# Optimization experiments

Hardware: AMD Instinct MI355X
Metric: run time of the kernel (lower is better)

Reference implementation:

```python
import jax, jax.numpy as jnp
import numpy as np

B, N, K = 64, 1024, 20
HEADS, DIM_K, DIM_V, CH_RAISE = 8, 32, 32, 64
C_CAT = 4 * 2 + DIM_V  # 44


def setup_inputs() -> dict:
    key = jax.random.key(0)
    ks = jax.random.split(key, 16)

    def w(k, shape):
        fan_in = shape[-1]
        return jax.random.normal(k, shape, dtype=jnp.float32) / np.sqrt(fan_in)

    def gamma(k, n):
        return 1.0 + 0.1 * jax.random.normal(k, (n,), dtype=jnp.float32)

    def beta(k, n):
        return 0.1 * jax.random.normal(k, (n,), dtype=jnp.float32)

    return {
        "x": jax.random.normal(ks[0], (B, N, 4), dtype=jnp.float32),
        "W_h": w(ks[1], (DIM_V, 4)),              # mlp_h: conv2d 4 -> dim_v, 1x1
        "W1": w(ks[2], (CH_RAISE, C_CAT)),        # mlp conv2d 44 -> 64
        "g1": gamma(ks[3], CH_RAISE), "b1": beta(ks[4], CH_RAISE),
        "W2": w(ks[5], (CH_RAISE, CH_RAISE)),     # mlp conv2d 64 -> 64
        "g2": gamma(ks[6], CH_RAISE), "b2": beta(ks[7], CH_RAISE),
        "W_v": w(ks[8], (DIM_V, C_CAT)),          # mlp_v conv1d 44 -> 32
        "gv": gamma(ks[9], DIM_V), "bv": beta(ks[10], DIM_V),
        "W_k": w(ks[11], (DIM_K, C_CAT)),         # mlp_k conv1d 44 -> 32
        "W_q": w(ks[12], (HEADS * DIM_K, CH_RAISE)),  # mlp_q conv1d 64 -> 256
        "gq": gamma(ks[13], HEADS * DIM_K), "bq": beta(ks[14], HEADS * DIM_K),
    }


def _forward(x, W_h, W1, g1, b1, W2, g2, b2, W_v, gv, bv, W_k, W_q, gq, bq):
    xyz = x[..., :4]                 # [B,N,4]
    feat = xyz                       # use_norm=False -> feature = xyz
    b, n, _ = xyz.shape

    # squared pairwise distances [B,N,N]
    sq = jnp.sum(xyz * xyz, axis=-1)
    dist = -2.0 * jnp.einsum('bnc,bmc->bnm', xyz, xyz) + sq[:, :, None] + sq[:, None, :]

    # KNN: K smallest distances
    _, knn_idx = jax.lax.top_k(-dist, K)          # [B,N,K]
    bidx = jnp.arange(b)[:, None, None]
    neighbor_xyz = xyz[bidx, knn_idx]             # [B,N,K,4]
    grouped = feat[bidx, knn_idx]                 # [B,N,K,4]

    feat_t = jnp.transpose(feat, (0, 2, 1))       # [B,4,N]
    grouped_c = jnp.transpose(grouped, (0, 3, 1, 2))          # [B,4,N,K]
    gnorm = grouped_c - feat_t[..., None]                     # [B,4,N,K]
    rel = jnp.transpose(neighbor_xyz - xyz[:, :, None, :], (0, 3, 1, 2))  # [B,4,N,K]

    pos = jnp.einsum('vc,bcnk->bvnk', W_h, rel)               # [B,32,N,K]
    center = jnp.broadcast_to(feat_t[..., None], (b, 4, n, K))
    feature = jnp.concatenate([gnorm, center, pos], axis=1)   # [B,44,N,K]

    # mlp: two 1x1 conv + BN(eval, affine) + ReLU
    h = jnp.einsum('oc,bcnk->bonk', W1, feature)
    h = jax.nn.relu(g1[None, :, None, None] * h + b1[None, :, None, None])
    h = jnp.einsum('oc,bcnk->bonk', W2, h)
    h = jax.nn.relu(g2[None, :, None, None] * h + b2[None, :, None, None])
    feature_q = jnp.max(h, axis=-1)                           # [B,64,N]

    q = jnp.einsum('oc,bcn->bon', W_q, feature_q)             # [B,256,N]
    q = jax.nn.relu(gq[None, :, None] * q + bq[None, :, None])
    q = q.reshape(b, HEADS, DIM_K, n)                         # [B,h,d,N]

    v = jnp.einsum('vc,bcnk->bvnk', W_v, feature)             # [B,32,N,K]
    v = gv[None, :, None, None] * v + bv[None, :, None, None]
    v = jnp.transpose(v, (0, 2, 1, 3))                        # [B,N,v,K]

    kk = jnp.einsum('dc,bcnk->bdnk', W_k, feature)            # [B,32,N,K]
    kk = jax.nn.softmax(kk, axis=-1)
    kk = jnp.transpose(kk, (0, 2, 1, 3))                      # [B,N,d,K]

    kv = jnp.einsum('bndk,bnvk->bdvn', kk, v)                 # [B,d,v,N]
    out = jnp.einsum('bhdn,bdvn->bhvn', q, kv)                # [B,h,v,N]
    out = out.reshape(b, HEADS * DIM_V, n)                    # [B,256,N]
    return xyz, out


def reference(x, W_h, W1, g1, b1, W2, g2, b2, W_v, gv, bv, W_k, W_q, gq, bq):
    return _forward(x, W_h, W1, g1, b1, W2, g2, b2, W_v, gv, bv, W_k, W_q, gq, bq)
```

## Files before the change

### kernel.cpp

```cpp
#include <hip/hip_runtime.h>
#include <math.h>

#define NPTS 1024
#define KNBR 20
#define CH 64


typedef __attribute__((ext_vector_type(8))) short s16x8;
typedef __attribute__((ext_vector_type(4))) float f32x4;

static __device__ __forceinline__ ushort f2bf(float f) {
  uint u = __float_as_uint(f);
  uint r = (u + 0x7FFFu + ((u >> 16) & 1u)) >> 16;
  return (ushort)r;
}

static __device__ __forceinline__ uint pkbf(float a, float b) {
  uint ua = __float_as_uint(a) + 0x8000u;
  uint ub = __float_as_uint(b) + 0x8000u;
  return __builtin_amdgcn_perm(ub, ua, 0x07060302);
}

static __device__ __forceinline__ int mbcnt64(unsigned long long m) {
  return __builtin_amdgcn_mbcnt_hi((uint)(m >> 32),
                                   __builtin_amdgcn_mbcnt_lo((uint)m, 0));
}

__global__ __launch_bounds__(256) void k_prep(
    const float* __restrict__ Wh, const float* __restrict__ W1,
    const float* __restrict__ g1, const float* __restrict__ b1,
    const float* __restrict__ Wv, const float* __restrict__ Wk,
    const float* __restrict__ W2, const float* __restrict__ Wq,
    float* __restrict__ wp, ushort* __restrict__ w2b,
    ushort* __restrict__ wqb, ushort* __restrict__ w1b) {
  int t = threadIdx.x;
  {
    int o = t >> 2, c = t & 3;
    float acc = W1[o * 40 + c];
    #pragma unroll
    for (int v = 0; v < 32; ++v) acc = fmaf(W1[o * 40 + 8 + v], Wh[v * 4 + c], acc);
    float g = g1[o];
    wp[t] = g * acc;
    wp[256 + t] = g * W1[o * 40 + 4 + c];
  }
  if (t < 128) {
    int d = t >> 2, c = t & 3;
    float av = Wv[d * 40 + c];
    float ak = Wk[d * 40 + c];
    #pragma unroll
    for (int u = 0; u < 32; ++u) {
      av = fmaf(Wv[d * 40 + 8 + u], Wh[u * 4 + c], av);
      ak = fmaf(Wk[d * 40 + 8 + u], Wh[u * 4 + c], ak);
    }
    wp[512 + t] = av;
    wp[640 + t] = Wv[d * 40 + 4 + c];
    wp[768 + t] = ak;
    wp[896 + t] = Wk[d * 40 + 4 + c];
  }
  #pragma unroll
  for (int i = 0; i < 16; ++i) w2b[t * 16 + i] = f2bf(W2[t * 16 + i]);
  for (int i = 0; i < 64; ++i) wqb[t * 64 + i] = f2bf(Wq[t * 64 + i]);
  __syncthreads();
  for (int idx = t; idx < 2048; idx += 256) {
    int ch = idx >> 5, kk = idx & 31;
    float v = 0.f;
    if (kk < 4) v = wp[ch * 4 + kk];
    else if (kk < 8) v = wp[256 + ch * 4 + (kk - 4)];
    else if (kk == 8) v = b1[ch];
    w1b[idx] = f2bf(v);
  }
}

__global__ __launch_bounds__(256) void k_knn(const float4* __restrict__ xv,
                                             ushort* __restrict__ knn,
                                             float4* __restrict__ outx) {
  __shared__ float4 sx[NPTS];
  __shared__ float ssq[NPTS];
  __shared__ uint s_sk[4][64];
  __shared__ ushort s_sj[4][64];

  int t = threadIdx.x;
  int b = blockIdx.x >> 6, grp = blockIdx.x & 63;
  for (int j = t; j < NPTS; j += 256) {
    float4 p = xv[b * NPTS + j];
    sx[j] = p;
    ssq[j] = p.x * p.x + p.y * p.y + p.z * p.z + p.w * p.w;
    if (grp == 0) outx[b * NPTS + j] = p;
  }
  __syncthreads();

  int w = t >> 6, l = t & 63;

  #pragma unroll 1
  for (int i = 0; i < 4; ++i) {
    int cloc = grp * 16 + w * 4 + i;
    int gid20 = (b * NPTS + cloc) * KNBR;
    float4 c = sx[cloc];
    uint u[16];
    uint mn = 0xFFFFFFFFu;
    #pragma unroll
    for (int s = 0; s < 16; ++s) {
      int j = s * 64 + l;
      float4 q = sx[j];
      float dot = c.x * q.x;
      dot = fmaf(c.y, q.y, dot);
      dot = fmaf(c.z, q.z, dot);
      dot = fmaf(c.w, q.w, dot);
      float key = fmaf(-2.f, dot, ssq[j]);
      uint uu = __float_as_uint(key);
      uu = ((int)uu < 0) ? ~uu : (uu | 0x80000000u);
      u[s] = uu;
      mn = min(mn, uu);
    }

    uint T0 = 0;
    #pragma unroll
    for (int bit = 31; bit >= 0; --bit) {
      uint cand = T0 | (1u << bit);
      if (__popcll(__ballot(mn < cand)) < 20) T0 = cand;
    }

    int base = 0;
    #pragma unroll
    for (int s = 0; s < 16; ++s) {
      unsigned long long mask = __ballot(u[s] <= T0);
      if (u[s] <= T0) {
        int off = base + mbcnt64(mask);
        if (off < 64) {
          s_sk[w][off] = u[s];
          s_sj[w][off] = (ushort)(s * 64 + l);
        }
      }
      base += (int)__popcll(mask);
    }
    int scnt = base;

    if (scnt <= 64) {
      asm volatile("s_waitcnt lgkmcnt(0)" ::: "memory");
      __builtin_amdgcn_sched_barrier(0);
      uint uk = (l < scnt) ? s_sk[w][l] : 0xFFFFFFFFu;
      uint uj = (l < scnt) ? (uint)s_sj[w][l] : 0xFFFFu;

      uint u20 = 0;
      #pragma unroll
      for (int bit = 31; bit >= 0; --bit) {
        uint cand = u20 | (1u << bit);
        if (__popcll(__ballot(uk < cand)) < 20) u20 = cand;
      }
      int m = (int)__popcll(__ballot(uk < u20));
      int r = 20 - m;
      uint jr = 0;
      #pragma unroll
      for (int bit = 10; bit >= 0; --bit) {
        uint cand = jr | (1u << bit);
        if (__popcll(__ballot((uk == u20) && (uj < cand))) < r) jr = cand;
      }
      bool sel = (uk < u20) || ((uk == u20) && (uj <= jr));
      unsigned long long smask = __ballot(sel);
      int off = mbcnt64(smask);
      if (sel) knn[gid20 + off] = (ushort)uj;
    } else {
      uint u20 = 0;
      #pragma unroll 1
      for (int bit = 31; bit >= 0; --bit) {
        uint cand = u20 | (1u << bit);
        int cnt2 = 0;
        #pragma unroll
        for (int s = 0; s < 16; ++s)
          cnt2 += (int)__popcll(__ballot(u[s] < cand));
        if (cnt2 < 20) u20 = cand;
      }
      int base2 = 0;
      #pragma unroll
      for (int s = 0; s < 16; ++s) {
        unsigned long long mask = __ballot(u[s] < u20);
        if (u[s] < u20) knn[gid20 + base2 + mbcnt64(mask)] = (ushort)(s * 64 + l);
        base2 += (int)__popcll(mask);
      }
      int r = 20 - base2;
      #pragma unroll
      for (int s = 0; s < 16; ++s) {
        unsigned long long mask = __ballot(u[s] == u20);
        int pos = mbcnt64(mask);
        int cntm = (int)__popcll(mask);
        int take = (r < cntm) ? r : cntm;
        if ((u[s] == u20) && (pos < take))
          knn[gid20 + base2 + pos] = (ushort)(s * 64 + l);
        base2 += take;
        r -= take;
      }
    }
  }
}

__global__ __launch_bounds__(256) void k_fused(
    const float4* __restrict__ xv, const ushort* __restrict__ knn,
    const float* __restrict__ wp, const ushort* __restrict__ w1b,
    const ushort* __restrict__ w2b, const ushort* __restrict__ wqb,
    const float* __restrict__ g2, const float* __restrict__ b2,
    const float* __restrict__ gq, const float* __restrict__ bq,
    const float* __restrict__ gv, const float* __restrict__ bv,
    float* __restrict__ o1) {
  __shared__ __align__(16) char smem[51200];
  char* s_h1 = smem;
  ushort* s_qb = (ushort*)smem;
  ushort* s_eb = (ushort*)(smem + 10496);
  float* s_out = (float*)(smem + 10496);
  float4* s_rel = (float4*)(smem + 40960);
  char* s_fqb = smem + 46080;
  float4* s_ctr = (float4*)(smem + 48384);
  ushort* s_ab = (ushort*)(smem + 40960);

  int t = threadIdx.x;
  int gid0 = blockIdx.x * 16;
  int bbase = (gid0 >> 10) << 10;
  int b = gid0 >> 10;
  int n0 = gid0 & 1023;
  int w = t >> 6, l = t & 63;
  int g = l >> 4, lane16 = l & 15;

  if (t < 16) s_ctr[t] = xv[gid0 + t];
  #pragma unroll
  for (int it2 = 0; it2 < 2; ++it2) {
    int idx = t + it2 * 256;
    if (idx < 320) {
      int p = (int)(((uint)idx * 3277u) >> 16);
      int k = idx - p * 20;
      int nb = (int)knn[(size_t)(gid0 + p) * KNBR + k];
      float4 nx = xv[bbase + nb];
      float4 ct = xv[gid0 + p];
      s_rel[p * 20 + k] =
          make_float4(nx.x - ct.x, nx.y - ct.y, nx.z - ct.z, nx.w - ct.w);
    }
  }
  __syncthreads();

  {
    s16x8 ah[4];
    #pragma unroll
    for (int m = 0; m < 4; ++m)
      ah[m] = *(const s16x8*)(w1b + (m * 16 + lane16) * 32 + g * 8);
    s16x8 bz = {0, 0, 0, 0, 0, 0, 0, 0};
    s16x8 bone = bz;
    bone[0] = (short)0x3F80;
    #pragma unroll
    for (int q = 0; q < 5; ++q) {
      int col = w * 80 + q * 16 + lane16;
      s16x8 bf;
      if (g == 0) {
        float4 r = s_rel[lane16 * 20 + 5 * w + q];
        float4 ct = s_ctr[lane16];
        union { uint4 u; s16x8 s; } cv;
        cv.u.x = pkbf(r.x, r.y);
        cv.u.y = pkbf(r.z, r.w);
        cv.u.z = pkbf(ct.x, ct.y);
        cv.u.w = pkbf(ct.z, ct.w);
        bf = cv.s;
      } else {
        bf = (g == 1) ? bone : bz;
      }
      int swz = (col & 7) << 4;
      #pragma unroll
      for (int m = 0; m < 4; ++m) {
        f32x4 acc = {0.f, 0.f, 0.f, 0.f};
        acc = __builtin_amdgcn_mfma_f32_16x16x32_bf16(ah[m], bf, acc, 0, 0, 0);
        uint2 hv;
        hv.x = pkbf(fmaxf(acc[0], 0.f), fmaxf(acc[1], 0.f));
        hv.y = pkbf(fmaxf(acc[2], 0.f), fmaxf(acc[3], 0.f));
        int byteoff = col * 128 + (m * 16 + g * 4) * 2;
        *(uint2*)(s_h1 + (byteoff ^ swz)) = hv;
      }
    }
  }
  __syncthreads();

  {
    int row0 = w * 16 + g * 4;
    s16x8 af0 = *(const s16x8*)(w2b + (w * 16 + lane16) * 64 + g * 8);
    s16x8 af1 = *(const s16x8*)(w2b + (w * 16 + lane16) * 64 + 32 + g * 8);
    float4 g2v = *(const float4*)(g2 + row0);
    float4 b2v = *(const float4*)(b2 + row0);
    float mx0 = 0.f, mx1 = 0.f, mx2 = 0.f, mx3 = 0.f;
    #pragma unroll 4
    for (int kt = 0; kt < 20; ++kt) {
      int col = kt * 16 + lane16;
      int rowbyte = col * 128;
      int swz = (col & 7) << 4;
      s16x8 bf0 = *(const s16x8*)(s_h1 + ((rowbyte + g * 16) ^ swz));
      s16x8 bf1 = *(const s16x8*)(s_h1 + ((rowbyte + 64 + g * 16) ^ swz));
      f32x4 acc = {0.f, 0.f, 0.f, 0.f};
      acc = __builtin_amdgcn_mfma_f32_16x16x32_bf16(af0, bf0, acc, 0, 0, 0);
      acc = __builtin_amdgcn_mfma_f32_16x16x32_bf16(af1, bf1, acc, 0, 0, 0);
      mx0 = fmaxf(mx0, fmaxf(fmaf(g2v.x, acc[0], b2v.x), 0.f));
      mx1 = fmaxf(mx1, fmaxf(fmaf(g2v.y, acc[1], b2v.y), 0.f));
      mx2 = fmaxf(mx2, fmaxf(fmaf(g2v.z, acc[2], b2v.z), 0.f));
      mx3 = fmaxf(mx3, fmaxf(fmaf(g2v.w, acc[3], b2v.w), 0.f));
    }
    uint2 u2;
    u2.x = pkbf(mx0, mx1);
    u2.y = pkbf(mx2, mx3);
    *(uint2*)(s_fqb + lane16 * 144 + row0 * 2) = u2;
  }
  __syncthreads();

  {
    s16x8 af[4][2];
    #pragma unroll
    for (int mm = 0; mm < 4; ++mm) {
      int row = w * 64 + mm * 16 + lane16;
      af[mm][0] = *(const s16x8*)(wqb + row * 64 + g * 8);
      af[mm][1] = *(const s16x8*)(wqb + row * 64 + 32 + g * 8);
    }
    s16x8 bf0 = *(const s16x8*)(s_fqb + lane16 * 144 + 0 * 64 + g * 16);
    s16x8 bf1 = *(const s16x8*)(s_fqb + lane16 * 144 + 1 * 64 + g * 16);
    #pragma unroll
    for (int mm = 0; mm < 4; ++mm) {
      f32x4 acc = {0.f, 0.f, 0.f, 0.f};
      acc = __builtin_amdgcn_mfma_f32_16x16x32_bf16(af[mm][0], bf0, acc, 0, 0, 0);
      acc = __builtin_amdgcn_mfma_f32_16x16x32_bf16(af[mm][1], bf1, acc, 0, 0, 0);
      int rbase = w * 64 + mm * 16 + g * 4;
      int h = rbase >> 5, d0 = rbase & 31;
      float4 gqv = *(const float4*)(gq + rbase);
      float4 bqv = *(const float4*)(bq + rbase);
      float v0 = fmaxf(fmaf(gqv.x, acc[0], bqv.x), 0.f);
      float v1 = fmaxf(fmaf(gqv.y, acc[1], bqv.y), 0.f);
      float v2 = fmaxf(fmaf(gqv.z, acc[2], bqv.z), 0.f);
      float v3 = fmaxf(fmaf(gqv.w, acc[3], bqv.w), 0.f);
      uint2 u2;
      u2.x = pkbf(v0, v1);
      u2.y = pkbf(v2, v3);
      *(uint2*)(s_qb + lane16 * 328 + h * 40 + d0) = u2;
    }
  }

  uint vp[2][10];
  {
    int d = t & 31, phalf = t >> 5;
    float4 wr = *(const float4*)(wp + 512 + 256 + d * 4);
    float4 wc = *(const float4*)(wp + 512 + 384 + d * 4);
    float4 vr_ = *(const float4*)(wp + 512 + 0 + d * 4);
    float4 vc_ = *(const float4*)(wp + 512 + 128 + d * 4);
    float gvd = gv[d], bvd = bv[d];
    #pragma unroll
    for (int i = 0; i < 2; ++i) {
      int p = phalf + 8 * i;
      float4 ct = s_ctr[p];
      float cb = fmaf(wc.x, ct.x, fmaf(wc.y, ct.y, fmaf(wc.z, ct.z, wc.w * ct.w)));
      float ev[KNBR];
      float sum = 0.f;
      #pragma unroll
      for (int k = 0; k < KNBR; ++k) {
        float4 r = s_rel[p * 20 + k];
        float kkv =
            fmaf(wr.x, r.x, fmaf(wr.y, r.y, fmaf(wr.z, r.z, fmaf(wr.w, r.w, cb))));
        ev[k] = __expf(kkv);
        sum += ev[k];
      }
      float cbv = fmaf(vc_.x, ct.x, fmaf(vc_.y, ct.y, fmaf(vc_.z, ct.z, vc_.w * ct.w)));
      float vv[KNBR];
      #pragma unroll
      for (int k = 0; k < KNBR; ++k) {
        float4 r = s_rel[p * 20 + k];
        float raw =
            fmaf(vr_.x, r.x, fmaf(vr_.y, r.y, fmaf(vr_.z, r.z, fmaf(vr_.w, r.w, cbv))));
        vv[k] = fmaf(gvd, raw, bvd);
      }
      float rs = 1.0f / sum;
      #pragma unroll
      for (int k = 0; k < KNBR; ++k)
        s_eb[(p * 20 + k) * 40 + d] = f2bf(ev[k] * rs);
      #pragma unroll
      for (int k2 = 0; k2 < 10; ++k2) vp[i][k2] = pkbf(vv[k2 * 2], vv[k2 * 2 + 1]);
    }
  }
  __syncthreads();

  #pragma unroll
  for (int pi2 = 0; pi2 < 4; ++pi2) {
    int plo = pi2 & 1, ii = pi2 >> 1;
    int pi = 2 * w + plo + 8 * ii;
    s16x8 qa = *(const s16x8*)(s_qb + pi * 328 + (lane16 & 7) * 40 + g * 8);
    #pragma unroll
    for (int tile = 0; tile < 2; ++tile) {
      int k = tile * 16 + lane16;
      int kc = (k < KNBR) ? k : (KNBR - 1);
      s16x8 eb = *(const s16x8*)(s_eb + (pi * 20 + kc) * 40 + g * 8);
      f32x4 acc = {0.f, 0.f, 0.f, 0.f};
      acc = __builtin_amdgcn_mfma_f32_16x16x32_bf16(qa, eb, acc, 0, 0, 0);
      if (g < 2) {
        if (k < KNBR) {
          #pragma unroll
          for (int r = 0; r < 4; ++r)
            s_ab[pi * 320 + (g * 4 + r) * 40 + k] = f2bf(acc[r]);
        } else {
          #pragma unroll
          for (int r = 0; r < 4; ++r) s_ab[pi * 320 + (g * 4 + r) * 40 + k] = 0;
        }
      }
    }
  }

  #pragma unroll
  for (int pi2 = 0; pi2 < 4; ++pi2) {
    int plo = pi2 & 1, ii = pi2 >> 1;
    int pi = 2 * w + plo + 8 * ii;
    s16x8 aa = *(const s16x8*)(s_ab + pi * 320 + (lane16 & 7) * 40 + g * 8);
    #pragma unroll
    for (int vt = 0; vt < 2; ++vt) {
      int srcl4 = ((plo * 32 + vt * 16 + lane16) << 2);
      uint bu[4];
      #pragma unroll
      for (int i = 0; i < 4; ++i) {
        uint t0 = (uint)__builtin_amdgcn_ds_bpermute(srcl4, (int)vp[ii][i]);
        uint t1 = (uint)__builtin_amdgcn_ds_bpermute(srcl4, (int)vp[ii][4 + i]);
        uint t2 = (i < 2)
                      ? (uint)__builtin_amdgcn_ds_bpermute(srcl4, (int)vp[ii][8 + i])
                      : 0u;
        bu[i] = (g == 0) ? t0 : (g == 1) ? t1 : (g == 2) ? t2 : 0u;
      }
      union { uint4 u; s16x8 s; } bb;
      bb.u.x = bu[0]; bb.u.y = bu[1]; bb.u.z = bu[2]; bb.u.w = bu[3];
      f32x4 acc = {0.f, 0.f, 0.f, 0.f};
      acc = __builtin_amdgcn_mfma_f32_16x16x32_bf16(aa, bb.s, acc, 0, 0, 0);
      if (g < 2) {
        int v = vt * 16 + lane16;
        #pragma unroll
        for (int r = 0; r < 4; ++r) {
          int h = g * 4 + r;
          s_out[(h * 32 + v) * 17 + pi] = acc[r];
        }
      }
    }
  }
  __syncthreads();

  #pragma unroll
  for (int e = 0; e < 16; ++e) {
    int idx = t + e * 256;
    int hv = idx >> 4, pp = idx & 15;
    o1[b * 262144 + hv * 1024 + n0 + pp] = s_out[hv * 17 + pp];
  }
}

extern "C" void kernel_launch(void* const* d_in, const int* in_sizes, int n_in,
                              void* d_out, int out_size, void* d_ws, size_t ws_size,
                              hipStream_t stream) {
  const float* x = (const float*)d_in[0];
  const float* Wh = (const float*)d_in[1];
  const float* W1 = (const float*)d_in[2];
  const float* g1 = (const float*)d_in[3];
  const float* b1 = (const float*)d_in[4];
  const float* W2 = (const float*)d_in[5];
  const float* g2 = (const float*)d_in[6];
  const float* b2 = (const float*)d_in[7];
  const float* Wv = (const float*)d_in[8];
  const float* gv = (const float*)d_in[9];
  const float* bv = (const float*)d_in[10];
  const float* Wk = (const float*)d_in[11];
  const float* Wq = (const float*)d_in[12];
  const float* gq = (const float*)d_in[13];
  const float* bq = (const float*)d_in[14];
  float* out = (float*)d_out;

  ushort* knn = (ushort*)d_ws;
  float* wp = (float*)((char*)d_ws + 19398656);
  ushort* w2b = (ushort*)((char*)d_ws + 19402752);
  ushort* wqb = (ushort*)((char*)d_ws + 19410944);
  ushort* w1b = (ushort*)((char*)d_ws + 19443712);

  hipLaunchKernelGGL(k_prep, dim3(1), dim3(256), 0, stream, Wh, W1, g1, b1, Wv, Wk,
                     W2, Wq, wp, w2b, wqb, w1b);
  hipLaunchKernelGGL(k_knn, dim3(4096), dim3(256), 0, stream, (const float4*)x, knn,
                     (float4*)out);
  hipLaunchKernelGGL(k_fused, dim3(4096), dim3(256), 0, stream, (const float4*)x,
                     knn, wp, w1b, w2b, wqb, g2, b2, gq, bq, gv, bv, out + 262144);
}
```

Measured before the change: 158.5 us.

## Fold weight prep into KNN kernel and interleave two-center radix selects

Removes the separate single-block weight-preparation launch by running that work inside block 1 of the KNN kernel, saving one kernel launch and its serialization gap. The KNN loop now handles two query points per iteration and interleaves their second-stage ballot-based radix selects, so independent ballots can overlap and hide latency. In exchange register pressure rises, and block 1 carries extra tail work.

```diff
diff --git a/kernel.cpp b/kernel.cpp
--- a/kernel.cpp
+++ b/kernel.cpp
@@ -26,54 +26,15 @@
                                    __builtin_amdgcn_mbcnt_lo((uint)m, 0));
 }
 
-__global__ __launch_bounds__(256) void k_prep(
-    const float* __restrict__ Wh, const float* __restrict__ W1,
-    const float* __restrict__ g1, const float* __restrict__ b1,
-    const float* __restrict__ Wv, const float* __restrict__ Wk,
-    const float* __restrict__ W2, const float* __restrict__ Wq,
-    float* __restrict__ wp, ushort* __restrict__ w2b,
-    ushort* __restrict__ wqb, ushort* __restrict__ w1b) {
-  int t = threadIdx.x;
-  {
-    int o = t >> 2, c = t & 3;
-    float acc = W1[o * 40 + c];
-    #pragma unroll
-    for (int v = 0; v < 32; ++v) acc = fmaf(W1[o * 40 + 8 + v], Wh[v * 4 + c], acc);
-    float g = g1[o];
-    wp[t] = g * acc;
-    wp[256 + t] = g * W1[o * 40 + 4 + c];
-  }
-  if (t < 128) {
-    int d = t >> 2, c = t & 3;
-    float av = Wv[d * 40 + c];
-    float ak = Wk[d * 40 + c];
-    #pragma unroll
-    for (int u = 0; u < 32; ++u) {
-      av = fmaf(Wv[d * 40 + 8 + u], Wh[u * 4 + c], av);
-      ak = fmaf(Wk[d * 40 + 8 + u], Wh[u * 4 + c], ak);
-    }
-    wp[512 + t] = av;
-    wp[640 + t] = Wv[d * 40 + 4 + c];
-    wp[768 + t] = ak;
-    wp[896 + t] = Wk[d * 40 + 4 + c];
-  }
-  #pragma unroll
-  for (int i = 0; i < 16; ++i) w2b[t * 16 + i] = f2bf(W2[t * 16 + i]);
-  for (int i = 0; i < 64; ++i) wqb[t * 64 + i] = f2bf(Wq[t * 64 + i]);
-  __syncthreads();
-  for (int idx = t; idx < 2048; idx += 256) {
-    int ch = idx >> 5, kk = idx & 31;
-    float v = 0.f;
-    if (kk < 4) v = wp[ch * 4 + kk];
-    else if (kk < 8) v = wp[256 + ch * 4 + (kk - 4)];
-    else if (kk == 8) v = b1[ch];
-    w1b[idx] = f2bf(v);
-  }
-}
-
-__global__ __launch_bounds__(256) void k_knn(const float4* __restrict__ xv,
-                                             ushort* __restrict__ knn,
-                                             float4* __restrict__ outx) {
+__global__ __launch_bounds__(256) void k_knn(
+    const float4* __restrict__ xv, ushort* __restrict__ knn,
+    float4* __restrict__ outx, const float* __restrict__ Wh,
+    const float* __restrict__ W1, const float* __restrict__ g1,
+    const float* __restrict__ b1, const float* __restrict__ Wv,
+    const float* __restrict__ Wk, const float* __restrict__ W2,
+    const float* __restrict__ Wq, float* __restrict__ wp,
+    ushort* __restrict__ w2b, ushort* __restrict__ wqb,
+    ushort* __restrict__ w1b) {
   __shared__ float4 sx[NPTS];
   __shared__ float ssq[NPTS];
   __shared__ uint s_sk[4][64];
@@ -92,103 +53,174 @@
   int w = t >> 6, l = t & 63;
 
   #pragma unroll 1
-  for (int i = 0; i < 4; ++i) {
-    int cloc = grp * 16 + w * 4 + i;
-    int gid20 = (b * NPTS + cloc) * KNBR;
-    float4 c = sx[cloc];
-    uint u[16];
-    uint mn = 0xFFFFFFFFu;
-    #pragma unroll
-    for (int s = 0; s < 16; ++s) {
-      int j = s * 64 + l;
-      float4 q = sx[j];
-      float dot = c.x * q.x;
-      dot = fmaf(c.y, q.y, dot);
-      dot = fmaf(c.z, q.z, dot);
-      dot = fmaf(c.w, q.w, dot);
-      float key = fmaf(-2.f, dot, ssq[j]);
-      uint uu = __float_as_uint(key);
-      uu = ((int)uu < 0) ? ~uu : (uu | 0x80000000u);
-      u[s] = uu;
-      mn = min(mn, uu);
-    }
-
-    uint T0 = 0;
+  for (int ip = 0; ip < 2; ++ip) {
+    int c0 = grp * 16 + w * 4 + ip * 2;
+    uint uk0 = 0xFFFFFFFFu, uj0 = 0xFFFFu, uk1 = 0xFFFFFFFFu, uj1 = 0xFFFFu;
+    bool done0 = false, done1 = false;
+
+    #pragma unroll
+    for (int cc = 0; cc < 2; ++cc) {
+      int cloc = c0 + cc;
+      int gid20 = (b * NPTS + cloc) * KNBR;
+      float4 c = sx[cloc];
+      uint u[16];
+      uint mn = 0xFFFFFFFFu;
+      #pragma unroll
+      for (int s = 0; s < 16; ++s) {
+        int j = s * 64 + l;
+        float4 q = sx[j];
+        float dot = c.x * q.x;
+        dot = fmaf(c.y, q.y, dot);
+        dot = fmaf(c.z, q.z, dot);
+        dot = fmaf(c.w, q.w, dot);
+        float key = fmaf(-2.f, dot, ssq[j]);
+        uint uu = __float_as_uint(key);
+        uu = ((int)uu < 0) ? ~uu : (uu | 0x80000000u);
+        u[s] = uu;
+        mn = min(mn, uu);
+      }
+
+      uint T0 = 0;
+      #pragma unroll
+      for (int bit = 31; bit >= 0; --bit) {
+        uint cand = T0 | (1u << bit);
+        if (__popcll(__ballot(mn < cand)) < 20) T0 = cand;
+      }
+
+      int base = 0;
+      #pragma unroll
+      for (int s = 0; s < 16; ++s) {
+        unsigned long long mask = __ballot(u[s] <= T0);
+        if (u[s] <= T0) {
+          int off = base + mbcnt64(mask);
+          if (off < 64) {
+            s_sk[w][off] = u[s];
+            s_sj[w][off] = (ushort)(s * 64 + l);
+          }
+        }
+        base += (int)__popcll(mask);
+      }
+      int scnt = base;
+
+      uint ukx, ujx;
+      bool donex = false;
+      if (scnt <= 64) {
+        asm volatile("s_waitcnt lgkmcnt(0)" ::: "memory");
+        __builtin_amdgcn_sched_barrier(0);
+        ukx = (l < scnt) ? s_sk[w][l] : 0xFFFFFFFFu;
+        ujx = (l < scnt) ? (uint)s_sj[w][l] : 0xFFFFu;
+      } else {
+        uint u20 = 0;
+        #pragma unroll 1
+        for (int bit = 31; bit >= 0; --bit) {
+          uint cand = u20 | (1u << bit);
+          int cnt2 = 0;
+          #pragma unroll
+          for (int s = 0; s < 16; ++s)
+            cnt2 += (int)__popcll(__ballot(u[s] < cand));
+          if (cnt2 < 20) u20 = cand;
+        }
+        int base2 = 0;
+        #pragma unroll
+        for (int s = 0; s < 16; ++s) {
+          unsigned long long mask = __ballot(u[s] < u20);
+          if (u[s] < u20)
+            knn[gid20 + base2 + mbcnt64(mask)] = (ushort)(s * 64 + l);
+          base2 += (int)__popcll(mask);
+        }
+        int r = 20 - base2;
+        #pragma unroll
+        for (int s = 0; s < 16; ++s) {
+          unsigned long long mask = __ballot(u[s] == u20);
+          int pos = mbcnt64(mask);
+          int cntm = (int)__popcll(mask);
+          int take = (r < cntm) ? r : cntm;
+          if ((u[s] == u20) && (pos < take))
+            knn[gid20 + base2 + pos] = (ushort)(s * 64 + l);
+          base2 += take;
+          r -= take;
+        }
+        donex = true;
+        ukx = 0xFFFFFFFFu;
+        ujx = 0xFFFFu;
+      }
+      if (cc == 0) {
+        uk0 = ukx; uj0 = ujx; done0 = donex;
+      } else {
+        uk1 = ukx; uj1 = ujx; done1 = donex;
+      }
+    }
+
+    uint u20a = 0, u20b = 0;
     #pragma unroll
     for (int bit = 31; bit >= 0; --bit) {
-      uint cand = T0 | (1u << bit);
-      if (__popcll(__ballot(mn < cand)) < 20) T0 = cand;
-    }
-
-    int base = 0;
-    #pragma unroll
-    for (int s = 0; s < 16; ++s) {
-      unsigned long long mask = __ballot(u[s] <= T0);
-      if (u[s] <= T0) {
-        int off = base + mbcnt64(mask);
-        if (off < 64) {
-          s_sk[w][off] = u[s];
-          s_sj[w][off] = (ushort)(s * 64 + l);
-        }
-      }
-      base += (int)__popcll(mask);
-    }
-    int scnt = base;
-
-    if (scnt <= 64) {
-      asm volatile("s_waitcnt lgkmcnt(0)" ::: "memory");
-      __builtin_amdgcn_sched_barrier(0);
-      uint uk = (l < scnt) ? s_sk[w][l] : 0xFFFFFFFFu;
-      uint uj = (l < scnt) ? (uint)s_sj[w][l] : 0xFFFFu;
-
-      uint u20 = 0;
-      #pragma unroll
-      for (int bit = 31; bit >= 0; --bit) {
-        uint cand = u20 | (1u << bit);
-        if (__popcll(__ballot(uk < cand)) < 20) u20 = cand;
-      }
-      int m = (int)__popcll(__ballot(uk < u20));
-      int r = 20 - m;
-      uint jr = 0;
-      #pragma unroll
-      for (int bit = 10; bit >= 0; --bit) {
-        uint cand = jr | (1u << bit);
-        if (__popcll(__ballot((uk == u20) && (uj < cand))) < r) jr = cand;
-      }
-      bool sel = (uk < u20) || ((uk == u20) && (uj <= jr));
-      unsigned long long smask = __ballot(sel);
-      int off = mbcnt64(smask);
-      if (sel) knn[gid20 + off] = (ushort)uj;
-    } else {
-      uint u20 = 0;
-      #pragma unroll 1
-      for (int bit = 31; bit >= 0; --bit) {
-        uint cand = u20 | (1u << bit);
-        int cnt2 = 0;
-        #pragma unroll
-        for (int s = 0; s < 16; ++s)
-          cnt2 += (int)__popcll(__ballot(u[s] < cand));
-        if (cnt2 < 20) u20 = cand;
-      }
-      int base2 = 0;
-      #pragma unroll
-      for (int s = 0; s < 16; ++s) {
-        unsigned long long mask = __ballot(u[s] < u20);
-        if (u[s] < u20) knn[gid20 + base2 + mbcnt64(mask)] = (ushort)(s * 64 + l);
-        base2 += (int)__popcll(mask);
-      }
-      int r = 20 - base2;
-      #pragma unroll
-      for (int s = 0; s < 16; ++s) {
-        unsigned long long mask = __ballot(u[s] == u20);
-        int pos = mbcnt64(mask);
-        int cntm = (int)__popcll(mask);
-        int take = (r < cntm) ? r : cntm;
-        if ((u[s] == u20) && (pos < take))
-          knn[gid20 + base2 + pos] = (ushort)(s * 64 + l);
-        base2 += take;
-        r -= take;
-      }
+      uint ca = u20a | (1u << bit);
+      uint cb = u20b | (1u << bit);
+      int na = (int)__popcll(__ballot(uk0 < ca));
+      int nb = (int)__popcll(__ballot(uk1 < cb));
+      if (na < 20) u20a = ca;
+      if (nb < 20) u20b = cb;
+    }
+    int ma = (int)__popcll(__ballot(uk0 < u20a));
+    int mb = (int)__popcll(__ballot(uk1 < u20b));
+    int ra = 20 - ma, rb = 20 - mb;
+    uint jra = 0, jrb = 0;
+    #pragma unroll
+    for (int bit = 10; bit >= 0; --bit) {
+      uint ca = jra | (1u << bit);
+      uint cb = jrb | (1u << bit);
+      int na = (int)__popcll(__ballot((uk0 == u20a) && (uj0 < ca)));
+      int nb = (int)__popcll(__ballot((uk1 == u20b) && (uj1 < cb)));
+      if (na < ra) jra = ca;
+      if (nb < rb) jrb = cb;
+    }
+    {
+      int gidA = (b * NPTS + c0) * KNBR;
+      bool selA = (uk0 < u20a) || ((uk0 == u20a) && (uj0 <= jra));
+      unsigned long long smA = __ballot(selA);
+      if (!done0 && selA) knn[gidA + mbcnt64(smA)] = (ushort)uj0;
+      bool selB = (uk1 < u20b) || ((uk1 == u20b) && (uj1 <= jrb));
+      unsigned long long smB = __ballot(selB);
+      if (!done1 && selB) knn[gidA + KNBR + mbcnt64(smB)] = (ushort)uj1;
+    }
+  }
+
+  if (blockIdx.x == 1) {
+    {
+      int o = t >> 2, c = t & 3;
+      float acc = W1[o * 40 + c];
+      #pragma unroll
+      for (int v = 0; v < 32; ++v)
+        acc = fmaf(W1[o * 40 + 8 + v], Wh[v * 4 + c], acc);
+      float g = g1[o];
+      wp[t] = g * acc;
+      wp[256 + t] = g * W1[o * 40 + 4 + c];
+    }
+    if (t < 128) {
+      int d = t >> 2, c = t & 3;
+      float av = Wv[d * 40 + c];
+      float ak = Wk[d * 40 + c];
+      #pragma unroll
+      for (int u2 = 0; u2 < 32; ++u2) {
+        av = fmaf(Wv[d * 40 + 8 + u2], Wh[u2 * 4 + c], av);
+        ak = fmaf(Wk[d * 40 + 8 + u2], Wh[u2 * 4 + c], ak);
+      }
+      wp[512 + t] = av;
+      wp[640 + t] = Wv[d * 40 + 4 + c];
+      wp[768 + t] = ak;
+      wp[896 + t] = Wk[d * 40 + 4 + c];
+    }
+    #pragma unroll
+    for (int i = 0; i < 16; ++i) w2b[t * 16 + i] = f2bf(W2[t * 16 + i]);
+    for (int i = 0; i < 64; ++i) wqb[t * 64 + i] = f2bf(Wq[t * 64 + i]);
+    __syncthreads();
+    for (int idx = t; idx < 2048; idx += 256) {
+      int ch = idx >> 5, kk = idx & 31;
+      float v = 0.f;
+      if (kk < 4) v = wp[ch * 4 + kk];
+      else if (kk < 8) v = wp[256 + ch * 4 + (kk - 4)];
+      else if (kk == 8) v = b1[ch];
+      w1b[idx] = f2bf(v);
     }
   }
 }
@@ -468,10 +500,9 @@
   ushort* wqb = (ushort*)((char*)d_ws + 19410944);
   ushort* w1b = (ushort*)((char*)d_ws + 19443712);
 
-  hipLaunchKernelGGL(k_prep, dim3(1), dim3(256), 0, stream, Wh, W1, g1, b1, Wv, Wk,
-                     W2, Wq, wp, w2b, wqb, w1b);
   hipLaunchKernelGGL(k_knn, dim3(4096), dim3(256), 0, stream, (const float4*)x, knn,
-                     (float4*)out);
+                     (float4*)out, Wh, W1, g1, b1, Wv, Wk, W2, Wq, wp, w2b, wqb,
+                     w1b);
   hipLaunchKernelGGL(k_fused, dim3(4096), dim3(256), 0, stream, (const float4*)x,
                      knn, wp, w1b, w2b, wqb, g2, b2, gq, bq, gv, bv, out + 262144);
 }
```

New measurement: 152.9 us (median of 2 runs). 1.04x faster.
